# Kernel optimization log

Hardware: AMD Instinct MI355X
Metric: run time of the kernel (lower is better)

## Reference

```python
import jax, jax.numpy as jnp
import numpy as np
from jax.ops import segment_sum

HIDDEN = 128  # hard-coded in VGAEModel.__init__


def gcn_conv(x, W, b, src, dst, n_nodes):
    """PyG GCNConv: h = x@W; add self-loops; symmetric norm D^-1/2 A D^-1/2; scatter-add; +bias."""
    h = x @ W  # [N, out]
    loop = jnp.arange(n_nodes, dtype=src.dtype)
    s = jnp.concatenate([src, loop])  # [E+N]
    d = jnp.concatenate([dst, loop])  # [E+N]
    deg = segment_sum(jnp.ones_like(d, dtype=h.dtype), d, num_segments=n_nodes)  # [N]
    dinv = jnp.where(deg > 0, jax.lax.rsqrt(deg), 0.0)
    norm = dinv[s] * dinv[d]  # [E+N]
    msg = h[s] * norm[:, None]  # [E+N, out] -- largest intermediate
    out = segment_sum(msg, d, num_segments=n_nodes)  # [N, out]
    return out + b


def setup_inputs() -> dict:
    key = jax.random.key(0)
    ks = jax.random.split(key, 8)
    N, E, IN, OUT = 50000, 1600000, 256, 64
    x = jax.random.normal(ks[0], (N, IN), dtype=jnp.float32)
    edge_index = jax.random.randint(ks[1], (2, E), 0, N, dtype=jnp.int32)
    sc = lambda fan_in: 1.0 / np.sqrt(fan_in)
    W1 = jax.random.uniform(ks[2], (IN, HIDDEN), jnp.float32, -sc(IN), sc(IN))
    b1 = jnp.zeros((HIDDEN,), jnp.float32)
    W_mu = jax.random.uniform(ks[3], (HIDDEN, OUT), jnp.float32, -sc(HIDDEN), sc(HIDDEN))
    b_mu = jnp.zeros((OUT,), jnp.float32)
    W_ls = jax.random.uniform(ks[4], (HIDDEN, OUT), jnp.float32, -sc(HIDDEN), sc(HIDDEN))
    b_ls = jnp.zeros((OUT,), jnp.float32)
    return {"x": x, "edge_index": edge_index, "n_nodes": N,
            "W1": W1, "b1": b1, "W_mu": W_mu, "b_mu": b_mu, "W_ls": W_ls, "b_ls": b_ls}


def reference(x, edge_index, n_nodes, W1, b1, W_mu, b_mu, W_ls, b_ls):
    src, dst = edge_index[0], edge_index[1]
    h = jax.nn.relu(gcn_conv(x, W1, b1, src, dst, n_nodes))
    mu = gcn_conv(h, W_mu, b_mu, src, dst, n_nodes)
    logstd = gcn_conv(h, W_ls, b_ls, src, dst, n_nodes)
    return (mu, logstd)
```

## Files before the change

### kernel.cpp

```cpp
#include <hip/hip_runtime.h>
#include <hip/hip_fp16.h>


#define IN_DIM 256
#define F1 128
#define F2 64
#define QF 32
#define BN 128
#define CAP 4736
#define BIN_EDGES 4096
#define SIDX 768

typedef _Float16 f16x8 __attribute__((ext_vector_type(8)));
typedef _Float16 f16x4 __attribute__((ext_vector_type(4)));
typedef float f32x4 __attribute__((ext_vector_type(4)));

static inline int cdiv_i(int a, int b) { return (a + b - 1) / b; }

__device__ static inline uint32_t lds_addr(const void* p) {
    return (uint32_t)(size_t)(const __attribute__((address_space(3))) void*)p;
}

__global__ void k_prep_frags(const float* __restrict__ W1,
                             const float* __restrict__ Wmu,
                             const float* __restrict__ Wls,
                             __half* __restrict__ W1frag,
                             __half* __restrict__ Wcfrag) {
    int t = blockIdx.x * blockDim.x + threadIdx.x;
    if (t < 8 * 8 * 64) {
        int lane = t & 63, nt = (t >> 6) & 7, ks = t >> 9;
        int k0 = ks * 32 + ((lane >> 4) << 3);
        int n = nt * 16 + (lane & 15);
#pragma unroll
        for (int j = 0; j < 8; ++j)
            W1frag[(size_t)t * 8 + j] = __float2half(W1[(k0 + j) * F1 + n]);
    } else if (t < 8 * 8 * 64 + 4 * 8 * 64) {
        int u = t - 8 * 8 * 64;
        int lane = u & 63, nt = (u >> 6) & 7, ks = u >> 9;
        int k0 = ks * 32 + ((lane >> 4) << 3);
        int c = nt * 16 + (lane & 15);
        const float* W = (c < F2) ? (Wmu + c) : (Wls + (c - F2));
#pragma unroll
        for (int j = 0; j < 8; ++j)
            Wcfrag[(size_t)u * 8 + j] = __float2half(W[(k0 + j) * F2]);
    }
}

__global__ __launch_bounds__(512) void k_binning(const int* __restrict__ src,
                                                 const int* __restrict__ dst,
                                                 int* __restrict__ bcur,
                                                 int* __restrict__ pairs, int E) {
    __shared__ int hcnt[512];
    __shared__ int hrank[512];
    __shared__ int hbase[512];
    __shared__ int lbase[512];
    __shared__ int stage[BIN_EDGES];
    __shared__ int gaddr[BIN_EDGES];
    const int tid = threadIdx.x;
    hcnt[tid] = 0; hrank[tid] = 0;
    __syncthreads();
    const int e0 = blockIdx.x * BIN_EDGES;
    int s_[8], d_[8];
#pragma unroll
    for (int it = 0; it < 8; ++it) {
        int e = e0 + it * 512 + tid;
        if (e < E) {
            s_[it] = src[e];
            d_[it] = dst[e];
            atomicAdd(&hcnt[d_[it] >> 7], 1);
        } else {
            d_[it] = -1;
        }
    }
    __syncthreads();
    int v = hcnt[tid];
    lbase[tid] = v;
    __syncthreads();
    for (int ofs = 1; ofs < 512; ofs <<= 1) {
        int add = (tid >= ofs) ? lbase[tid - ofs] : 0;
        __syncthreads();
        lbase[tid] += add;
        __syncthreads();
    }
    int total = lbase[511];
    int excl = lbase[tid] - v;
    __syncthreads();
    lbase[tid] = excl;
    hbase[tid] = v ? atomicAdd(&bcur[tid], v) : 0;
    __syncthreads();
#pragma unroll
    for (int it = 0; it < 8; ++it) {
        if (d_[it] >= 0) {
            int b = d_[it] >> 7;
            int r = atomicAdd(&hrank[b], 1);
            int li = lbase[b] + r;
            stage[li] = ((d_[it] & (BN - 1)) << 16) | s_[it];
            gaddr[li] = b * CAP + hbase[b] + r;
        }
    }
    __syncthreads();
    for (int i = tid; i < total; i += 512)
        pairs[gaddr[i]] = stage[i];
}

__global__ __launch_bounds__(512) void k_bucket_build(const int* __restrict__ pairs,
                                                      const int* __restrict__ bcur,
                                                      float* __restrict__ dinv,
                                                      int* __restrict__ rs,
                                                      int* __restrict__ re,
                                                      int* __restrict__ ssrc, int N) {
    __shared__ int hist[BN];
    __shared__ int offs[BN];
    __shared__ int stage[CAP];
    const int b = blockIdx.x;
    const int n0 = b * BN;
    const int tid = threadIdx.x;
    const int pbase = b * CAP;
    const int cnt = min(bcur[b], CAP);
    if (tid < BN) hist[tid] = 0;
    __syncthreads();
    for (int e = tid; e < cnt; e += 512)
        atomicAdd(&hist[pairs[pbase + e] >> 16], 1);
    __syncthreads();
    if (tid < BN) offs[tid] = hist[tid];
    __syncthreads();
    for (int ofs = 1; ofs < BN; ofs <<= 1) {
        int add = 0;
        if (tid < BN && tid >= ofs) add = offs[tid - ofs];
        __syncthreads();
        if (tid < BN) offs[tid] += add;
        __syncthreads();
    }
    if (tid < BN) {
        int incl = offs[tid];
        int excl = incl - hist[tid];
        int n = n0 + tid;
        if (n < N) {
            dinv[n] = rsqrtf((float)hist[tid] + 1.0f);
            rs[n] = pbase + excl;
            re[n] = pbase + incl;
        }
        offs[tid] = excl;
    }
    __syncthreads();
    for (int e = tid; e < cnt; e += 512) {
        int p = pairs[pbase + e];
        int idx = atomicAdd(&offs[p >> 16], 1);
        stage[idx] = p & 0xFFFF;
    }
    __syncthreads();
    for (int i = tid; i < cnt; i += 512) ssrc[pbase + i] = stage[i];
}

__global__ __launch_bounds__(256) void k_gemm1_mfma(const float* __restrict__ x,
                                                    const __half* __restrict__ W1frag,
                                                    const float* __restrict__ dinv,
                                                    __half* __restrict__ C, int M) {
    const int wave = threadIdx.x >> 6;
    const int lane = threadIdx.x & 63;
    const int m0 = blockIdx.x * 64 + wave * 16;
    if (m0 >= M) return;
    const int q = lane >> 4;
    const int arow = m0 + (lane & 15);
    f32x4 acc[8] = {};
#pragma unroll
    for (int ks = 0; ks < 8; ++ks) {
        const float* ap = x + (size_t)arow * IN_DIM + ks * 32 + q * 8;
        f32x4 f0 = *(const f32x4*)(ap);
        f32x4 f1 = *(const f32x4*)(ap + 4);
        f16x8 a = { (_Float16)f0.x, (_Float16)f0.y, (_Float16)f0.z, (_Float16)f0.w,
                    (_Float16)f1.x, (_Float16)f1.y, (_Float16)f1.z, (_Float16)f1.w };
        const __half* bbase = W1frag + ((size_t)(ks * 8) * 64 + lane) * 8;
#pragma unroll
        for (int nt = 0; nt < 8; ++nt) {
            f16x8 bfrag = *(const f16x8*)(bbase + (size_t)nt * 64 * 8);
            acc[nt] = __builtin_amdgcn_mfma_f32_16x16x32_f16(a, bfrag, acc[nt], 0, 0, 0);
        }
    }
    float dv[4];
#pragma unroll
    for (int r = 0; r < 4; ++r) dv[r] = dinv[m0 + q * 4 + r];
#pragma unroll
    for (int nt = 0; nt < 8; ++nt) {
        int col = nt * 16 + (lane & 15);
        __half* cq = C + (size_t)(col >> 5) * M * QF + (col & 31);
#pragma unroll
        for (int r = 0; r < 4; ++r)
            cq[(size_t)(m0 + q * 4 + r) * QF] = __float2half(acc[nt][r] * dv[r]);
    }
}

__global__ __launch_bounds__(256) void k_gemm2_mfma(const __half* __restrict__ A,
                                                    const __half* __restrict__ Wcfrag,
                                                    const float* __restrict__ dinv,
                                                    __half* __restrict__ C, int M) {
    const int wave = threadIdx.x >> 6;
    const int lane = threadIdx.x & 63;
    const int m0 = blockIdx.x * 64 + wave * 16;
    if (m0 >= M) return;
    const int q = lane >> 4;
    const int arow = m0 + (lane & 15);
    f32x4 acc[8] = {};
#pragma unroll
    for (int ks = 0; ks < 4; ++ks) {
        f16x8 a = *(const f16x8*)(A + (size_t)ks * M * QF + (size_t)arow * QF + q * 8);
        const __half* bbase = Wcfrag + ((size_t)(ks * 8) * 64 + lane) * 8;
#pragma unroll
        for (int nt = 0; nt < 8; ++nt) {
            f16x8 bfrag = *(const f16x8*)(bbase + (size_t)nt * 64 * 8);
            acc[nt] = __builtin_amdgcn_mfma_f32_16x16x32_f16(a, bfrag, acc[nt], 0, 0, 0);
        }
    }
    float dv[4];
#pragma unroll
    for (int r = 0; r < 4; ++r) dv[r] = dinv[m0 + q * 4 + r];
#pragma unroll
    for (int nt = 0; nt < 8; ++nt) {
        int col = nt * 16 + (lane & 15);
        __half* cq = C + (size_t)(col >> 5) * M * QF + (col & 31);
#pragma unroll
        for (int r = 0; r < 4; ++r)
            cq[(size_t)(m0 + q * 4 + r) * QF] = __float2half(acc[nt][r] * dv[r]);
    }
}

#define ISSUE4(C_, LB, SA, SB)                                                 \
    {                                                                          \
        const int ebA_ = gs + (C_) * 32 + e4;                                  \
        const int ebB_ = ebA_ + 16;                                            \
        const __half* gpA_ = (ebA_ < ge)                                       \
            ? (tq + (size_t)(SA) * QF + b8) : (zrow + b8);                     \
        const __half* gpB_ = (ebB_ < ge)                                       \
            ? (tq + (size_t)(SB) * QF + b8) : (zrow + b8);                     \
        __builtin_amdgcn_global_load_lds(                                      \
            (const __attribute__((address_space(1))) void*)gpA_,               \
            (__attribute__((address_space(3))) void*)(LB), 16, 0, 0);          \
        __builtin_amdgcn_global_load_lds(                                      \
            (const __attribute__((address_space(1))) void*)gpB_,               \
            (__attribute__((address_space(3))) void*)((LB) + 512), 16, 0, 0);  \
    }

template<bool FIRST>
__global__ __launch_bounds__(256) void k_gather_mfma(
        const int* __restrict__ rs, const int* __restrict__ re,
        const int* __restrict__ ssrc, const float* __restrict__ dinv,
        const __half* __restrict__ t, const __half* __restrict__ zrow,
        const float* __restrict__ bA, const float* __restrict__ bB,
        __half* __restrict__ h, float* __restrict__ out,
        int N, int NG) {
    __shared__ __align__(16) __half smem[4][2][1024];
    __shared__ __align__(16) int    sidx[4][SIDX];
    const int wave = threadIdx.x >> 6;
    const int lane = threadIdx.x & 63;
    const int x = blockIdx.x & 7;
    const int q = x >> 1;
    const int g = (((blockIdx.x >> 3) << 1) + (x & 1)) * 4 + wave;
    if (g >= NG) return;
    const int nb = g << 4;
    const int e4 = lane >> 2;
    const int b8 = (lane & 3) * 8;
    const int col = lane & 15;
    const __half* tq = t + (size_t)q * N * QF;
    __half* buf0 = &smem[wave][0][0];
    __half* buf1 = &smem[wave][1][0];
    int* sb = &sidx[wave][0];
    const int o0 = rs[nb + col];
    const int o1 = re[nb + col];
    const int gs = rs[nb];
    const int ge = re[nb + 15];
    const int ne = ge - gs;
    const int nc = (ne + 31) >> 5;
    const int m0 = (lane >> 4) << 2;
    const int ebase = gs + m0 - o0;
    const unsigned dd = (unsigned)(o1 - o0);
    const uint32_t voff = 256u * (lane >> 4) + 64u * ((lane >> 2) & 3)
                        + 8u * (lane & 3);
    const uint32_t va0 = lds_addr(buf0) + voff;
    const uint32_t va1 = lds_addr(buf1) + voff;
    f32x4 acc0 = {}, acc1 = {};

    auto getsv = [&](int C, int& A_, int& B_) {
        int ia = C * 32 + e4;
        if (C < SIDX / 32) {
            A_ = sb[ia];
            B_ = sb[ia + 16];
        } else {
            int cap = ne > 0 ? ne - 1 : 0;
            A_ = ssrc[gs + min(ia, cap)];
            B_ = ssrc[gs + min(ia + 16, cap)];
        }
    };

    if (nc > 0) {
        const int nblk = min((ne + 255) >> 8, SIDX / 256);
        for (int b = 0; b < nblk; ++b)
            __builtin_amdgcn_global_load_lds(
                (const __attribute__((address_space(1))) void*)(ssrc + gs + b * 256 + lane * 4),
                (__attribute__((address_space(3))) void*)(sb + b * 256), 16, 0, 0);
        asm volatile("s_waitcnt vmcnt(0)" ::: "memory");
        int svA, svB;
        getsv(0, svA, svB);
        ISSUE4(0, buf0, svA, svB);
        getsv(1, svA, svB);
        for (int c = 0; c < nc; ++c) {
            if (c + 1 < nc) {
                ISSUE4(c + 1, (c & 1) ? buf0 : buf1, svA, svB);
                getsv(c + 2, svA, svB);
                asm volatile("s_waitcnt vmcnt(2)" ::: "memory");
            } else {
                asm volatile("s_waitcnt vmcnt(0)" ::: "memory");
            }
            const uint32_t va = (c & 1) ? va1 : va0;
            f16x4 r0, r1, r2, r3;
            asm volatile(
                "ds_read_b64_tr_b16 %0, %4 offset:0\n\t"
                "ds_read_b64_tr_b16 %1, %4 offset:1024\n\t"
                "ds_read_b64_tr_b16 %2, %4 offset:32\n\t"
                "ds_read_b64_tr_b16 %3, %4 offset:1056\n\t"
                "s_waitcnt lgkmcnt(0)"
                : "=&v"(r0), "=&v"(r1), "=&v"(r2), "=&v"(r3)
                : "v"(va) : "memory");
            __builtin_amdgcn_sched_barrier(0);
            f16x8 bf0, bf1;
#pragma unroll
            for (int j = 0; j < 4; ++j) {
                bf0[j] = r0[j]; bf0[j + 4] = r1[j];
                bf1[j] = r2[j]; bf1[j + 4] = r3[j];
            }
            const int eb = ebase + c * 32;
            f16x8 af;
#pragma unroll
            for (int j = 0; j < 8; ++j) {
                int m = eb + (j & 3) + ((j >> 2) << 4);
                af[j] = ((unsigned)m < dd) ? (_Float16)1.0f : (_Float16)0.0f;
            }
            acc0 = __builtin_amdgcn_mfma_f32_16x16x32_f16(af, bf0, acc0, 0, 0, 0);
            acc1 = __builtin_amdgcn_mfma_f32_16x16x32_f16(af, bf1, acc1, 0, 0, 0);
        }
    }
    const int nl0 = (lane >> 4) << 2;
#pragma unroll
    for (int r2 = 0; r2 < 4; ++r2) {
        const int node = nb + nl0 + r2;
        const float di = dinv[node];
        const float s0 = __half2float(tq[(size_t)node * QF + col]);
        const float s1 = __half2float(tq[(size_t)node * QF + 16 + col]);
        float v0 = (acc0[r2] + s0) * di;
        float v1 = (acc1[r2] + s1) * di;
        if constexpr (FIRST) {
            v0 += bA[q * QF + col];
            v1 += bA[q * QF + 16 + col];
            _Float16* hp = (_Float16*)(h + (size_t)q * N * QF + (size_t)node * QF);
            __builtin_nontemporal_store((_Float16)fmaxf(v0, 0.f), hp + col);
            __builtin_nontemporal_store((_Float16)fmaxf(v1, 0.f), hp + 16 + col);
        } else {
            const float* bp = (q < 2) ? bA : bB;
            const int fb = (q & 1) * QF;
            v0 += bp[fb + col];
            v1 += bp[fb + 16 + col];
            float* op = (q < 2) ? (out + (size_t)node * F2 + fb)
                                : (out + (size_t)N * F2 + (size_t)node * F2 + fb);
            __builtin_nontemporal_store(v0, op + col);
            __builtin_nontemporal_store(v1, op + 16 + col);
        }
    }
}

extern "C" void kernel_launch(void* const* d_in, const int* in_sizes, int n_in,
                              void* d_out, int out_size, void* d_ws, size_t ws_size,
                              hipStream_t stream) {
    const float* x   = (const float*)d_in[0];
    const int*   ei  = (const int*)d_in[1];
    const float* W1  = (const float*)d_in[3];
    const float* b1  = (const float*)d_in[4];
    const float* Wmu = (const float*)d_in[5];
    const float* bmu = (const float*)d_in[6];
    const float* Wls = (const float*)d_in[7];
    const float* bls = (const float*)d_in[8];

    const int N = in_sizes[0] / IN_DIM;
    const int E = in_sizes[1] / 2;
    const int* src = ei;
    const int* dst = ei + E;
    float* out = (float*)d_out;
    const int nbuck = cdiv_i(N, BN);

    size_t off = 0;
    auto carve = [&](size_t n) { size_t o = off; off += (n + 3) & ~(size_t)3; return o; };
    float* ws = (float*)d_ws;
    float*  dinv   =        ws + carve(N);
    int*    rs     = (int*)(ws + carve(N));
    int*    re     = (int*)(ws + carve(N));
    int*    bcur   = (int*)(ws + carve(512));
    __half* zrow   = (__half*)(ws + carve(16));
    int*    ssrc   = (int*)(ws + carve((size_t)nbuck * CAP + 256));
    __half* t16    = (__half*)(ws + carve((size_t)N * F1 / 2));
    __half* h16    = (__half*)(ws + carve((size_t)N * F1 / 2));
    __half* W1frag = (__half*)(ws + carve(8 * 8 * 64 * 8 / 2));
    __half* Wcfrag = (__half*)(ws + carve(4 * 8 * 64 * 8 / 2));
    (void)ws_size;
    int* pairs = (int*)t16;
    __half* t2_16 = t16;

    k_prep_frags<<<cdiv_i(8 * 8 * 64 + 4 * 8 * 64, 256), 256, 0, stream>>>(
        W1, Wmu, Wls, W1frag, Wcfrag);

    hipMemsetAsync(bcur, 0, sizeof(int) * 512 + 64, stream);
    k_binning<<<cdiv_i(E, BIN_EDGES), 512, 0, stream>>>(src, dst, bcur, pairs, E);
    k_bucket_build<<<nbuck, 512, 0, stream>>>(pairs, bcur, dinv, rs, re, ssrc, N);

    const int NG = N >> 4;
    const int NBI = cdiv_i(NG, 8);

    k_gemm1_mfma<<<cdiv_i(N, 64), 256, 0, stream>>>(x, W1frag, dinv, t16, N);
    k_gather_mfma<true><<<8 * NBI, 256, 0, stream>>>(
        rs, re, ssrc, dinv, t16, zrow, b1, b1, h16, out, N, NG);
    k_gemm2_mfma<<<cdiv_i(N, 64), 256, 0, stream>>>(h16, Wcfrag, dinv, t2_16, N);
    k_gather_mfma<false><<<8 * NBI, 256, 0, stream>>>(
        rs, re, ssrc, dinv, t2_16, zrow, bmu, bls, h16, out, N, NG);
}
```

Measured before the change: 246.5 us.

## Deepen gather pipeline to four stages, store source indices as u16, swizzle LDS

Stores the sorted per-bucket source indices as 16-bit values instead of 32-bit, halving index traffic and letting a larger index window fit in LDS. The gather kernel moves from a double buffer to a four-slot ring with three chunks in flight, and adjusts the vmcnt waits to match. It also XOR-swizzles the LDS staging layout so the transposed reads hit fewer bank conflicts. LDS use per block grows, which may lower occupancy, and the u16 indices assume node ids within a bucket segment fit in 16 bits.

```diff
diff --git a/kernel.cpp b/kernel.cpp
--- a/kernel.cpp
+++ b/kernel.cpp
@@ -9,7 +9,8 @@
 #define BN 128
 #define CAP 4736
 #define BIN_EDGES 4096
-#define SIDX 768
+#define SIDW 1024
+#define SBLK 512
 
 typedef _Float16 f16x8 __attribute__((ext_vector_type(8)));
 typedef _Float16 f16x4 __attribute__((ext_vector_type(4)));
@@ -108,7 +109,7 @@
                                                       float* __restrict__ dinv,
                                                       int* __restrict__ rs,
                                                       int* __restrict__ re,
-                                                      int* __restrict__ ssrc, int N) {
+                                                      ushort* __restrict__ ssrc, int N) {
     __shared__ int hist[BN];
     __shared__ int offs[BN];
     __shared__ int stage[CAP];
@@ -149,7 +150,8 @@
         stage[idx] = p & 0xFFFF;
     }
     __syncthreads();
-    for (int i = tid; i < cnt; i += 512) ssrc[pbase + i] = stage[i];
+    for (int i = tid; i < cnt; i += 512)
+        ssrc[pbase + i] = (ushort)stage[i];
 }
 
 __global__ __launch_bounds__(256) void k_gemm1_mfma(const float* __restrict__ x,
@@ -229,9 +231,9 @@
         const int ebA_ = gs + (C_) * 32 + e4;                                  \
         const int ebB_ = ebA_ + 16;                                            \
         const __half* gpA_ = (ebA_ < ge)                                       \
-            ? (tq + (size_t)(SA) * QF + b8) : (zrow + b8);                     \
+            ? (tq + (size_t)(SA) * QF + b8s) : (zrow + b8s);                   \
         const __half* gpB_ = (ebB_ < ge)                                       \
-            ? (tq + (size_t)(SB) * QF + b8) : (zrow + b8);                     \
+            ? (tq + (size_t)(SB) * QF + b8s) : (zrow + b8s);                   \
         __builtin_amdgcn_global_load_lds(                                      \
             (const __attribute__((address_space(1))) void*)gpA_,               \
             (__attribute__((address_space(3))) void*)(LB), 16, 0, 0);          \
@@ -243,13 +245,13 @@
 template<bool FIRST>
 __global__ __launch_bounds__(256) void k_gather_mfma(
         const int* __restrict__ rs, const int* __restrict__ re,
-        const int* __restrict__ ssrc, const float* __restrict__ dinv,
+        const ushort* __restrict__ ssrc, const float* __restrict__ dinv,
         const __half* __restrict__ t, const __half* __restrict__ zrow,
         const float* __restrict__ bA, const float* __restrict__ bB,
         __half* __restrict__ h, float* __restrict__ out,
         int N, int NG) {
-    __shared__ __align__(16) __half smem[4][2][1024];
-    __shared__ __align__(16) int    sidx[4][SIDX];
+    __shared__ __align__(16) __half  smem[4][4][1024];
+    __shared__ __align__(16) ushort  sidx[4][SIDW];
     const int wave = threadIdx.x >> 6;
     const int lane = threadIdx.x & 63;
     const int x = blockIdx.x & 7;
@@ -258,12 +260,11 @@
     if (g >= NG) return;
     const int nb = g << 4;
     const int e4 = lane >> 2;
-    const int b8 = (lane & 3) * 8;
+    const int b8s = (8 * (lane & 3)) ^ (((lane >> 3) & 1) << 4);
     const int col = lane & 15;
     const __half* tq = t + (size_t)q * N * QF;
-    __half* buf0 = &smem[wave][0][0];
-    __half* buf1 = &smem[wave][1][0];
-    int* sb = &sidx[wave][0];
+    __half* stg = &smem[wave][0][0];
+    ushort* sb = &sidx[wave][0];
     const int o0 = rs[nb + col];
     const int o1 = re[nb + col];
     const int gs = rs[nb];
@@ -273,17 +274,20 @@
     const int m0 = (lane >> 4) << 2;
     const int ebase = gs + m0 - o0;
     const unsigned dd = (unsigned)(o1 - o0);
-    const uint32_t voff = 256u * (lane >> 4) + 64u * ((lane >> 2) & 3)
-                        + 8u * (lane & 3);
-    const uint32_t va0 = lds_addr(buf0) + voff;
-    const uint32_t va1 = lds_addr(buf1) + voff;
+    const int u_ = (lane >> 2) & 3;
+    const uint32_t voff = 256u * (uint32_t)(lane >> 4) + 64u * (uint32_t)u_
+                        + 8u * (uint32_t)(lane & 3);
+    const uint32_t vaL = lds_addr(stg) + (voff ^ (uint32_t)((u_ & 2) << 4));
     f32x4 acc0 = {}, acc1 = {};
+
+    const int gsa = gs & ~7;
+    const int ofs = gs - gsa;
 
     auto getsv = [&](int C, int& A_, int& B_) {
         int ia = C * 32 + e4;
-        if (C < SIDX / 32) {
-            A_ = sb[ia];
-            B_ = sb[ia + 16];
+        if (ofs + C * 32 + 32 <= SIDW) {
+            A_ = sb[ofs + ia];
+            B_ = sb[ofs + ia + 16];
         } else {
             int cap = ne > 0 ? ne - 1 : 0;
             A_ = ssrc[gs + min(ia, cap)];
@@ -292,34 +296,42 @@
     };
 
     if (nc > 0) {
-        const int nblk = min((ne + 255) >> 8, SIDX / 256);
+        const int nblk = min((ofs + ne + SBLK - 1) / SBLK, SIDW / SBLK);
         for (int b = 0; b < nblk; ++b)
             __builtin_amdgcn_global_load_lds(
-                (const __attribute__((address_space(1))) void*)(ssrc + gs + b * 256 + lane * 4),
-                (__attribute__((address_space(3))) void*)(sb + b * 256), 16, 0, 0);
+                (const __attribute__((address_space(1))) void*)(ssrc + gsa + b * SBLK + lane * 8),
+                (__attribute__((address_space(3))) void*)(sb + b * SBLK), 16, 0, 0);
         asm volatile("s_waitcnt vmcnt(0)" ::: "memory");
         int svA, svB;
-        getsv(0, svA, svB);
-        ISSUE4(0, buf0, svA, svB);
-        getsv(1, svA, svB);
+        const int pre = min(nc, 3);
+        for (int p = 0; p < pre; ++p) {
+            getsv(p, svA, svB);
+            ISSUE4(p, stg + (p << 10), svA, svB);
+        }
+        getsv(3, svA, svB);
         for (int c = 0; c < nc; ++c) {
-            if (c + 1 < nc) {
-                ISSUE4(c + 1, (c & 1) ? buf0 : buf1, svA, svB);
-                getsv(c + 2, svA, svB);
-                asm volatile("s_waitcnt vmcnt(2)" ::: "memory");
+            const int jn = c + 3;
+            if (jn < nc) {
+                ISSUE4(jn, stg + ((jn & 3) << 10), svA, svB);
+                getsv(jn + 1, svA, svB);
+                asm volatile("s_waitcnt vmcnt(6)" ::: "memory");
             } else {
-                asm volatile("s_waitcnt vmcnt(0)" ::: "memory");
+                const int rem = nc - 1 - c;
+                if (rem >= 2)      asm volatile("s_waitcnt vmcnt(4)" ::: "memory");
+                else if (rem == 1) asm volatile("s_waitcnt vmcnt(2)" ::: "memory");
+                else               asm volatile("s_waitcnt vmcnt(0)" ::: "memory");
             }
-            const uint32_t va = (c & 1) ? va1 : va0;
+            const uint32_t vaLc = vaL + ((uint32_t)(c & 3) << 11);
+            const uint32_t vaHc = vaLc ^ 32u;
             f16x4 r0, r1, r2, r3;
             asm volatile(
                 "ds_read_b64_tr_b16 %0, %4 offset:0\n\t"
                 "ds_read_b64_tr_b16 %1, %4 offset:1024\n\t"
-                "ds_read_b64_tr_b16 %2, %4 offset:32\n\t"
-                "ds_read_b64_tr_b16 %3, %4 offset:1056\n\t"
+                "ds_read_b64_tr_b16 %2, %5 offset:0\n\t"
+                "ds_read_b64_tr_b16 %3, %5 offset:1024\n\t"
                 "s_waitcnt lgkmcnt(0)"
                 : "=&v"(r0), "=&v"(r1), "=&v"(r2), "=&v"(r3)
-                : "v"(va) : "memory");
+                : "v"(vaLc), "v"(vaHc) : "memory");
             __builtin_amdgcn_sched_barrier(0);
             f16x8 bf0, bf1;
 #pragma unroll
@@ -393,7 +405,7 @@
     int*    re     = (int*)(ws + carve(N));
     int*    bcur   = (int*)(ws + carve(512));
     __half* zrow   = (__half*)(ws + carve(16));
-    int*    ssrc   = (int*)(ws + carve((size_t)nbuck * CAP + 256));
+    ushort* ssrc   = (ushort*)(ws + carve(((size_t)nbuck * CAP + 1024) / 2));
     __half* t16    = (__half*)(ws + carve((size_t)N * F1 / 2));
     __half* h16    = (__half*)(ws + carve((size_t)N * F1 / 2));
     __half* W1frag = (__half*)(ws + carve(8 * 8 * 64 * 8 / 2));
```

Result: no change. 244.5 us (-0.8%).
